# Optimization experiments

Measured on AMD Instinct MI355X. Metric: run time of the kernel, lower is better.

## Reference

```python
import jax, jax.numpy as jnp
import numpy as np

RCUT = 6.0      # cutoff radius
AXIS = 16       # axis_neuron
NORM = 64.0     # normalizer = avg_neighbors + 1 (precomputed stat)
EPS = 1e-15
NTYPES = 2


def _embed(h, W0, b0, W1, b1, W2, b2):
    # tiny per-type-pair embedding MLP: scalar sr -> C channels
    h = jnp.tanh(h @ W0 + b0)
    h = jnp.tanh(h @ W1 + b1)
    return jnp.tanh(h @ W2 + b2)


def _forward(coord_3N, box_33, srmean, srstd, xrsrstd, Gbias, Ebias,
             emb_W0, emb_b0, emb_W1, emb_b1, emb_W2, emb_b2,
             fit_W0, fit_b0, fit_W1, fit_b1, fit_W2, fit_b2, n1):
    N = coord_3N.shape[1]
    L = jnp.diagonal(box_33)  # orthorhombic box lengths (3,)
    # relative coords with minimum-image convention: x[d,i,j] = c[d,j] - c[d,i]
    x_3NM = coord_3N[:, None, :] - coord_3N[:, :, None]
    x_3NM = x_3NM - L[:, None, None] * jnp.round(x_3NM / L[:, None, None])
    eye = jnp.eye(N, dtype=bool)
    r_NM = jnp.sqrt(jnp.where(eye, 1.0, (x_3NM ** 2).sum(0)))  # diag masked for safe grad
    # smooth switching / r  (DeepPot-SE style sr)
    u = r_NM / RCUT
    sw = jnp.where((r_NM < RCUT) & (~eye), ((-6.0 * u + 15.0) * u - 10.0) * u ** 3 + 1.0, 0.0)
    sr_NM = sw / r_NM
    rsr_NM = sr_NM / r_NM
    idx = (0, n1, N)  # contiguous type boundaries (atoms sorted by type)
    rows_sr, rows_rsr, rows_emb = [], [], []
    for i in range(NTYPES):
        sr_i = sr_NM[idx[i]:idx[i + 1]]
        rows_sr.append(sr_i / srstd[i])
        rows_rsr.append(rsr_NM[idx[i]:idx[i + 1]] / xrsrstd[i])
        srn_i = (sr_i - srmean[i]) / srstd[i]
        blocks = []
        for j in range(NTYPES):
            p = NTYPES * i + j  # type-pair index
            blocks.append(_embed(srn_i[:, idx[j]:idx[j + 1], None],
                                 emb_W0[p], emb_b0[p], emb_W1[p], emb_b1[p], emb_W2[p], emb_b2[p]))
        rows_emb.append(jnp.concatenate(blocks, axis=1))
    srbias_NM = jnp.concatenate(rows_sr, axis=0)
    R_3NM = (jnp.concatenate(rows_rsr, axis=0)[None] + EPS) * x_3NM  # e3norm = 1
    embed_NMC = jnp.concatenate(rows_emb, axis=0)
    # weighted reductions over neighbor axis M (einsum avoids the 3*N*M*C temp)
    Ginv_NC = jnp.einsum('nm,nmc->nc', srbias_NM, embed_NMC) / NORM
    Geqv_3NC = jnp.einsum('dnm,nmc->dnc', R_3NM, embed_NMC) / NORM
    G_4NC = jnp.concatenate([(Ginv_NC + Gbias)[None], Geqv_3NC], axis=0)
    # equivariant outer-product descriptor: Feat[n,a,c] = sum_k G[k,n,c]*G[k,n,a]
    Feat_NX = jnp.einsum('knc,kna->nac', G_4NC, G_4NC[:, :, :AXIS]).reshape(N, -1)
    energy = jnp.zeros((), dtype=Feat_NX.dtype)
    for i in range(NTYPES):
        h = Feat_NX[idx[i]:idx[i + 1]]
        h = jnp.tanh(h @ fit_W0[i] + fit_b0[i])
        h = jnp.tanh(h @ fit_W1[i] + fit_b1[i])
        h = h @ fit_W2[i] + fit_b2[i]
        energy = energy + (h + Ebias[i]).sum()
    return energy


def setup_inputs() -> dict:
    key = jax.random.key(0)
    ks = jax.random.split(key, 20)
    N, N1, BOXL = 1024, 512, 20.0
    W = (16, 32, 64)
    X, F = AXIS * W[-1], 128

    def wt(k, shape, fan_in):
        return jax.random.normal(k, shape, jnp.float32) / np.float32(np.sqrt(fan_in))

    return {
        'coord_3N': jax.random.uniform(ks[0], (3, N), jnp.float32) * BOXL,
        'box_33': BOXL * jnp.eye(3, dtype=jnp.float32),
        'srmean': 0.1 * jax.random.uniform(ks[1], (NTYPES,), jnp.float32),
        'srstd': 0.5 + jax.random.uniform(ks[2], (NTYPES,), jnp.float32),
        'xrsrstd': 0.5 + jax.random.uniform(ks[3], (NTYPES,), jnp.float32),
        'Gbias': 0.1 * jax.random.normal(ks[4], (W[2],), jnp.float32),
        'Ebias': jax.random.normal(ks[5], (NTYPES,), jnp.float32),
        'emb_W0': wt(ks[6], (4, 1, W[0]), 1),
        'emb_b0': 0.1 * jax.random.normal(ks[7], (4, W[0]), jnp.float32),
        'emb_W1': wt(ks[8], (4, W[0], W[1]), W[0]),
        'emb_b1': 0.1 * jax.random.normal(ks[9], (4, W[1]), jnp.float32),
        'emb_W2': wt(ks[10], (4, W[1], W[2]), W[1]),
        'emb_b2': 0.1 * jax.random.normal(ks[11], (4, W[2]), jnp.float32),
        'fit_W0': wt(ks[12], (NTYPES, X, F), X),
        'fit_b0': 0.1 * jax.random.normal(ks[13], (NTYPES, F), jnp.float32),
        'fit_W1': wt(ks[14], (NTYPES, F, F), F),
        'fit_b1': 0.1 * jax.random.normal(ks[15], (NTYPES, F), jnp.float32),
        'fit_W2': wt(ks[16], (NTYPES, F, 1), F),
        'fit_b2': 0.1 * jax.random.normal(ks[17], (NTYPES, 1), jnp.float32),
        'n1': N1,
    }


def reference(coord_3N, box_33, srmean, srstd, xrsrstd, Gbias, Ebias,
              emb_W0, emb_b0, emb_W1, emb_b1, emb_W2, emb_b2,
              fit_W0, fit_b0, fit_W1, fit_b1, fit_W2, fit_b2, n1):
    return _forward(coord_3N, box_33, srmean, srstd, xrsrstd, Gbias, Ebias,
                    emb_W0, emb_b0, emb_W1, emb_b1, emb_W2, emb_b2,
                    fit_W0, fit_b0, fit_W1, fit_b1, fit_W2, fit_b2, n1)
```

## Files before the change

### kernel.cpp

```cpp
#include <hip/hip_runtime.h>

#define RCUT 6.0f

typedef _Float16 h2v __attribute__((ext_vector_type(2)));
typedef _Float16 h8  __attribute__((ext_vector_type(8)));
typedef float    f4  __attribute__((ext_vector_type(4)));

__device__ __forceinline__ float fast_tanh(float x) {
    float e = __expf(2.0f * x);
    return 1.0f - 2.0f * __builtin_amdgcn_rcpf(e + 1.0f);
}

__device__ __forceinline__ h2v pkh(float a, float b) {
#if __has_builtin(__builtin_amdgcn_cvt_pkrtz)
    union { __fp16 __attribute__((ext_vector_type(2))) r; h2v h; } u;
    u.r = __builtin_amdgcn_cvt_pkrtz(a, b);
    return u.h;
#else
    h2v r; r.x = (_Float16)a; r.y = (_Float16)b; return r;
#endif
}

__global__ __launch_bounds__(256, 3) void k_embed(
    const float* __restrict__ coord, const float* __restrict__ box,
    const float* __restrict__ srmean, const float* __restrict__ srstd,
    const float* __restrict__ xrsrstd, const float* __restrict__ Gbias,
    const float* __restrict__ eW0, const float* __restrict__ eb0,
    const float* __restrict__ eW1, const float* __restrict__ eb1,
    const float* __restrict__ eW2, const float* __restrict__ eb2,
    const int* __restrict__ n1p,
    const float* __restrict__ fW0, const float* __restrict__ fW1,
    h2v* __restrict__ feat, _Float16* __restrict__ W0ht,
    _Float16* __restrict__ W1ht, unsigned int* __restrict__ counter, int N)
{
    const int nb  = blockIdx.x;
    const int tid = threadIdx.x;
    const int NB  = N >> 1;

    __shared__ float s_w0[2][16], s_b0[2][16];
    __shared__ __align__(16) _Float16 s_srn[1024];
    __shared__ __align__(16) _Float16 s_cf[4][1024];
    __shared__ __align__(16) _Float16 s_h1[128][32];
    __shared__ __align__(16) _Float16 s_ef[4][4][64][8];
    __shared__ unsigned short s_nbr[1024];
    __shared__ float s_g4[2][256];
    __shared__ __align__(16) _Float16 w1t[2][32][24];
    __shared__ __align__(16) _Float16 w2t[2][64][40];
    __shared__ int s_wA[4], s_wB[4];

    if (nb >= NB) {
        const int b = nb - NB;
        if (b == 0 && tid == 0) *counter = 0u;
        float (*s_t)[33] = reinterpret_cast<float(*)[33]>(&s_ef[0][0][0][0]);
        if (b < 256) {
            int type = b >> 7, tb = b & 127;
            int ki = tb >> 2, ci = tb & 3;
            const float* src = fW0 + (size_t)type * 131072;
            int c = tid & 31, r0 = (tid >> 5) * 4;
            #pragma unroll
            for (int q = 0; q < 4; q++)
                s_t[r0 + q][c] = src[(size_t)(ki * 32 + r0 + q) * 128 + ci * 32 + c];
            __syncthreads();
            _Float16* dst = W0ht + (size_t)type * 131072;
            int kk = tid & 31, c0 = (tid >> 5) * 4;
            #pragma unroll
            for (int q = 0; q < 4; q++)
                dst[(size_t)(ci * 32 + c0 + q) * 1024 + ki * 32 + kk] = (_Float16)s_t[kk][c0 + q];
        } else {
            int b2v = b - 256, type = b2v >> 4, tb = b2v & 15;
            int ki = tb >> 2, ci = tb & 3;
            const float* src = fW1 + (size_t)type * 16384;
            int c = tid & 31, r0 = (tid >> 5) * 4;
            #pragma unroll
            for (int q = 0; q < 4; q++)
                s_t[r0 + q][c] = src[(size_t)(ki * 32 + r0 + q) * 128 + ci * 32 + c];
            __syncthreads();
            _Float16* dst = W1ht + (size_t)type * 16384;
            int kk = tid & 31, c0 = (tid >> 5) * 4;
            #pragma unroll
            for (int q = 0; q < 4; q++)
                dst[(size_t)(ci * 32 + c0 + q) * 128 + ki * 32 + kk] = (_Float16)s_t[kk][c0 + q];
        }
        return;
    }

    const int nA = 2 * nb, nBt = 2 * nb + 1;
    const int n1 = *n1p;
    const int ti = (nA >= n1) ? 1 : 0;
    const int wid = tid >> 6, lane = tid & 63;
    const int l15 = lane & 15, lk = lane >> 4;

    for (int t = tid; t < 32; t += 256) { int j = t >> 4, f = t & 15;
        s_w0[j][f] = eW0[(2 * ti + j) * 16 + f];
        s_b0[j][f] = eb0[(2 * ti + j) * 16 + f]; }
    for (int idx = tid; idx < 1024; idx += 256) {
        int j = idx >> 9, r = idx & 511, f = r >> 5, g = r & 31;
        w1t[j][g][f] = (_Float16)eW1[(2 * ti + j) * 512 + f * 32 + g];
    }
    for (int idx = tid; idx < 4096; idx += 256) {
        int j = idx >> 11, r = idx & 2047, g = r >> 6, c = r & 63;
        w2t[j][c][g] = (_Float16)eW2[(2 * ti + j) * 2048 + g * 64 + c];
    }
    float b1r[2][2], b2r[2][4];
    #pragma unroll
    for (int j = 0; j < 2; j++) {
        #pragma unroll
        for (int q = 0; q < 2; q++) b1r[j][q] = eb1[(2 * ti + j) * 32 + 16 * q + l15];
        #pragma unroll
        for (int q = 0; q < 4; q++) b2r[j][q] = eb2[(2 * ti + j) * 64 + 16 * q + l15];
    }

    const float Lx = box[0], Ly = box[4], Lz = box[8];
    const float iLx = 1.0f / Lx, iLy = 1.0f / Ly, iLz = 1.0f / Lz;
    const float xA = coord[nA], yA = coord[N + nA], zA = coord[2 * N + nA];
    const float xB = coord[nBt], yB = coord[N + nBt], zB = coord[2 * N + nBt];
    const float srm  = srmean[ti];
    const float isrs = 1.0f / srstd[ti];
    const float ixrs = 1.0f / xrsrstd[ti];

    unsigned long long balA[4], balB[4];
    float dxA[4], dyA[4], dzA[4], r2A[4];
    float dxB[4], dyB[4], dzB[4], r2B[4];
    {
        int wA = 0, wB = 0;
        const int mystart = wid * 256;
        #pragma unroll
        for (int r = 0; r < 4; r++) {
            int m = mystart + r * 64 + lane;
            float x = coord[m], y = coord[N + m], z = coord[2 * N + m];
            float ax = x - xA; ax -= Lx * rintf(ax * iLx);
            float ay = y - yA; ay -= Ly * rintf(ay * iLy);
            float az = z - zA; az -= Lz * rintf(az * iLz);
            float ra = ax * ax + ay * ay + az * az;
            float bx = x - xB; bx -= Lx * rintf(bx * iLx);
            float by = y - yB; by -= Ly * rintf(by * iLy);
            float bz = z - zB; bz -= Lz * rintf(bz * iLz);
            float rb = bx * bx + by * by + bz * bz;
            dxA[r] = ax; dyA[r] = ay; dzA[r] = az; r2A[r] = ra;
            dxB[r] = bx; dyB[r] = by; dzB[r] = bz; r2B[r] = rb;
            bool pA = (ra < RCUT * RCUT) && (m != nA);
            bool pB = (rb < RCUT * RCUT) && (m != nBt);
            balA[r] = __ballot(pA);
            balB[r] = __ballot(pB);
            wA += (int)__popcll(balA[r]);
            wB += (int)__popcll(balB[r]);
        }
        if (lane == 0) { s_wA[wid] = wA; s_wB[wid] = wB; }
    }
    __syncthreads();
    int cntA = s_wA[0] + s_wA[1] + s_wA[2] + s_wA[3];
    int cntB = s_wB[0] + s_wB[1] + s_wB[2] + s_wB[3];
    int cnt  = cntA + cntB;
    if (cnt > 1024) cnt = 1024;
    if (cntA > 1024) cntA = 1024;
    {
        int baseA = 0, baseB = cntA;
        for (int w = 0; w < wid; w++) { baseA += s_wA[w]; baseB += s_wB[w]; }
        const unsigned long long lt = (1ull << lane) - 1ull;
        const int mystart = wid * 256;
        #pragma unroll
        for (int r = 0; r < 4; r++) {
            int m = mystart + r * 64 + lane;
            #pragma unroll
            for (int cc = 0; cc < 2; cc++) {
                unsigned long long bal = cc ? balB[r] : balA[r];
                int base = cc ? baseB : baseA;
                if ((bal >> lane) & 1ull) {
                    int pos = base + (int)__popcll(bal & lt);
                    if (pos < 1024) {
                        float dx = cc ? dxB[r] : dxA[r];
                        float dy = cc ? dyB[r] : dyA[r];
                        float dz = cc ? dzB[r] : dzA[r];
                        float r2 = cc ? r2B[r] : r2A[r];
                        float rr = sqrtf(r2);
                        float rinv = __builtin_amdgcn_rcpf(rr);
                        float u  = rr * (1.0f / RCUT);
                        float u3 = u * u * u;
                        float sw_ = ((-6.0f * u + 15.0f) * u - 10.0f) * u3 + 1.0f;
                        float sr  = sw_ * rinv;
                        float crs = sr * rinv * ixrs + 1e-15f;
                        s_srn[pos]   = (_Float16)((sr - srm) * isrs);
                        s_cf[0][pos] = (_Float16)(sr * isrs);
                        s_cf[1][pos] = (_Float16)(crs * dx);
                        s_cf[2][pos] = (_Float16)(crs * dy);
                        s_cf[3][pos] = (_Float16)(crs * dz);
                        s_nbr[pos]   = (unsigned short)m;
                    }
                }
                if (cc) baseB += (int)__popcll(bal);
                else    baseA += (int)__popcll(bal);
            }
        }
    }
    __syncthreads();
    const int ntiles = (cnt + 127) >> 7;
    for (int i = cnt + tid; i < ntiles * 128; i += 256) {
        s_srn[i] = (_Float16)0.0f; s_nbr[i] = 0;
        s_cf[0][i] = (_Float16)0.0f; s_cf[1][i] = (_Float16)0.0f;
        s_cf[2][i] = (_Float16)0.0f; s_cf[3][i] = (_Float16)0.0f;
    }
    __syncthreads();

    f4 gacc = {0.0f, 0.0f, 0.0f, 0.0f};
    const f4 zf4 = {0.0f, 0.0f, 0.0f, 0.0f};

    for (int t = 0; t < ntiles; t++) {
        const int t128 = t << 7;
        __syncthreads();

        #pragma unroll
        for (int mt2 = 0; mt2 < 2; mt2++) {
            const int mt = 2 * wid + mt2;
            const int row = 16 * mt + l15;
            const int rp = t128 + row;
            float srn = (float)s_srn[rp];
            int jr = (s_nbr[rp] >= n1) ? 1 : 0;
            h8 a = {};
            if (lk < 2) {
                const float* wp = &s_w0[jr][8 * lk];
                const float* bp = &s_b0[jr][8 * lk];
                #pragma unroll
                for (int q = 0; q < 8; q++)
                    a[q] = (_Float16)fast_tanh(fmaf(srn, wp[q], bp[q]));
            }
            #pragma unroll
            for (int nt1 = 0; nt1 < 2; nt1++) {
                const int c = 16 * nt1 + l15;
                h8 b0f = {}, b1f = {};
                if (lk < 2) {
                    b0f = *(const h8*)&w1t[0][c][8 * lk];
                    b1f = *(const h8*)&w1t[1][c][8 * lk];
                }
                f4 d0 = __builtin_amdgcn_mfma_f32_16x16x32_f16(a, b0f, zf4, 0, 0, 0);
                f4 d1 = __builtin_amdgcn_mfma_f32_16x16x32_f16(a, b1f, zf4, 0, 0, 0);
                #pragma unroll
                for (int r = 0; r < 4; r++) {
                    int gp = 16 * mt + 4 * lk + r;
                    bool is0 = (s_nbr[t128 + gp] < n1);
                    float hv = fast_tanh((is0 ? d0[r] : d1[r]) + (is0 ? b1r[0][nt1] : b1r[1][nt1]));
                    int e = 16 * nt1 + l15;
                    s_h1[gp][(((e >> 3) ^ ((gp >> 1) & 3)) << 3) + (e & 7)] = (_Float16)hv;
                }
            }
        }
        asm volatile("" ::: "memory");
        #pragma unroll
        for (int mt2 = 0; mt2 < 2; mt2++) {
            const int mt = 2 * wid + mt2;
            const int row = 16 * mt + l15;
            h8 a2 = *(const h8*)&s_h1[row][((lk ^ ((row >> 1) & 3)) << 3)];
            #pragma unroll
            for (int nt = 0; nt < 4; nt++) {
                const int c = 16 * nt + l15;
                h8 w20 = *(const h8*)&w2t[0][c][8 * lk];
                h8 w21 = *(const h8*)&w2t[1][c][8 * lk];
                f4 e0 = __builtin_amdgcn_mfma_f32_16x16x32_f16(a2, w20, zf4, 0, 0, 0);
                f4 e1 = __builtin_amdgcn_mfma_f32_16x16x32_f16(a2, w21, zf4, 0, 0, 0);
                #pragma unroll
                for (int r = 0; r < 4; r++) {
                    int gp = 16 * mt + 4 * lk + r;
                    bool is0 = (s_nbr[t128 + gp] < n1);
                    float ev = fast_tanh((is0 ? e0[r] : e1[r]) + (is0 ? b2r[0][nt] : b2r[1][nt]));
                    s_ef[nt][gp >> 5][l15 + 16 * ((gp & 31) >> 3)][gp & 7] = (_Float16)ev;
                }
            }
        }
        __syncthreads();

        #pragma unroll
        for (int ks = 0; ks < 4; ks++) {
            const int s = t128 + 32 * ks;
            h8 ac = {};
            if (l15 < 8) {
                const bool rowA = l15 < 4;
                const int  cr   = rowA ? l15 : (l15 - 4);
                const bool allA = (s + 31) < cntA;
                const bool allB = s >= cntA;
                if ((allA && rowA) || (allB && !rowA)) {
                    ac = *(const h8*)&s_cf[cr][s + 8 * lk];
                } else if (!allA && !allB) {
                    #pragma unroll
                    for (int r = 0; r < 8; r++) {
                        int p = s + 8 * lk + r;
                        bool isA = p < cntA;
                        if (isA == rowA) ac[r] = s_cf[cr][p];
                    }
                }
            }
            h8 eb = *(const h8*)&s_ef[wid][ks][lane][0];
            gacc = __builtin_amdgcn_mfma_f32_16x16x32_f16(ac, eb, gacc, 0, 0, 0);
        }
    }

    if (lk < 2) {
        float* sg = &s_g4[lk][0];
        #pragma unroll
        for (int r = 0; r < 4; r++) {
            float gv = gacc[r] * (1.0f / 64.0f);
            if (r == 0) gv += Gbias[16 * wid + l15];
            sg[r * 64 + 16 * wid + l15] = gv;
        }
    }
    __syncthreads();
    #pragma unroll
    for (int at = 0; at < 2; at++) {
        const float* sg = &s_g4[at][0];
        h2v* outp = feat + (size_t)(2 * nb + at) * 512;
        #pragma unroll
        for (int q = 0; q < 2; q++) {
            int o2 = tid + 256 * q;
            int a = o2 >> 5, c = (2 * o2) & 63;
            float ga0 = sg[a],       ga1 = sg[64 + a];
            float ga2 = sg[128 + a], ga3 = sg[192 + a];
            float s0 = ga0 * sg[c];
            s0 = fmaf(ga1, sg[64 + c],  s0);
            s0 = fmaf(ga2, sg[128 + c], s0);
            s0 = fmaf(ga3, sg[192 + c], s0);
            float s1 = ga0 * sg[c + 1];
            s1 = fmaf(ga1, sg[64 + c + 1],  s1);
            s1 = fmaf(ga2, sg[128 + c + 1], s1);
            s1 = fmaf(ga3, sg[192 + c + 1], s1);
            outp[o2] = pkh(s0, s1);
        }
    }
}

__global__ __launch_bounds__(512, 1) void k_fit(
    const _Float16* __restrict__ featf, const _Float16* __restrict__ W0ht,
    const _Float16* __restrict__ W1ht,
    const float* __restrict__ b0, const float* __restrict__ b1,
    const float* __restrict__ W2, const float* __restrict__ b2,
    const float* __restrict__ Ebias, const int* __restrict__ n1p,
    unsigned int* __restrict__ counter, float* __restrict__ slots,
    float* __restrict__ out)
{
    __shared__ float s_red[4][2][16][64];
    __shared__ __align__(16) _Float16 s_hd[16][128];
    __shared__ float s_sum[16][32];

    const int tid = threadIdx.x;
    const int lane = tid & 63, w = tid >> 6;
    const int kq = w >> 1, ch = w & 1;
    const int l15 = lane & 15, lk = lane >> 4;
    const int n0 = blockIdx.x * 16;
    const int ia = (n0 >= *n1p) ? 1 : 0;
    const f4 zf4 = {0.0f, 0.0f, 0.0f, 0.0f};

    const _Float16* Ap = featf + (size_t)(n0 + l15) * 1024 + kq * 256;
    const _Float16* B0 = W0ht + (size_t)ia * 131072 + kq * 256;
    f4 acc[4] = {zf4, zf4, zf4, zf4};
    #pragma unroll
    for (int ks = 0; ks < 8; ks++) {
        h8 a = *(const h8*)(Ap + ks * 32 + 8 * lk);
        #pragma unroll
        for (int nt = 0; nt < 4; nt++) {
            const int c = ch * 64 + nt * 16 + l15;
            h8 b = *(const h8*)(B0 + (size_t)c * 1024 + ks * 32 + 8 * lk);
            acc[nt] = __builtin_amdgcn_mfma_f32_16x16x32_f16(a, b, acc[nt], 0, 0, 0);
        }
    }
    #pragma unroll
    for (int nt = 0; nt < 4; nt++)
        #pragma unroll
        for (int r = 0; r < 4; r++)
            s_red[kq][ch][4 * lk + r][nt * 16 + l15] = acc[nt][r];
    __syncthreads();

    {
        const int row = tid >> 5, c0 = (tid & 31) * 4;
        const int chh = c0 >> 6, cl = c0 & 63;
        f4 v = *(const f4*)&s_red[0][chh][row][cl];
        v += *(const f4*)&s_red[1][chh][row][cl];
        v += *(const f4*)&s_red[2][chh][row][cl];
        v += *(const f4*)&s_red[3][chh][row][cl];
        #pragma unroll
        for (int q = 0; q < 4; q++) {
            int c = c0 + q;
            float h = fast_tanh(v[q] + b0[ia * 128 + c]);
            s_hd[row][(((c >> 3) ^ row) << 3) + (c & 7)] = (_Float16)h;
        }
    }
    __syncthreads();

    f4 acc1[4] = {zf4, zf4, zf4, zf4};
    {
        h8 a = *(const h8*)&s_hd[l15][(((4 * kq + lk) ^ l15) & 15) << 3];
        const _Float16* B1 = W1ht + (size_t)ia * 16384 + kq * 32;
        #pragma unroll
        for (int nt = 0; nt < 4; nt++) {
            const int c = ch * 64 + nt * 16 + l15;
            h8 b = *(const h8*)(B1 + (size_t)c * 128 + 8 * lk);
            acc1[nt] = __builtin_amdgcn_mfma_f32_16x16x32_f16(a, b, zf4, 0, 0, 0);
        }
    }
    #pragma unroll
    for (int nt = 0; nt < 4; nt++)
        #pragma unroll
        for (int r = 0; r < 4; r++)
            s_red[kq][ch][4 * lk + r][nt * 16 + l15] = acc1[nt][r];
    __syncthreads();

    {
        const int row = tid >> 5, c0 = (tid & 31) * 4;
        const int chh = c0 >> 6, cl = c0 & 63;
        f4 v = *(const f4*)&s_red[0][chh][row][cl];
        v += *(const f4*)&s_red[1][chh][row][cl];
        v += *(const f4*)&s_red[2][chh][row][cl];
        v += *(const f4*)&s_red[3][chh][row][cl];
        float pv = 0.0f;
        #pragma unroll
        for (int q = 0; q < 4; q++) {
            int c = c0 + q;
            pv += fast_tanh(v[q] + b1[ia * 128 + c]) * W2[ia * 128 + c];
        }
        s_sum[row][tid & 31] = pv;
    }
    __syncthreads();
    if (w == 0) {
        const int row = lane >> 2, g = lane & 3;
        float s = 0.0f;
        #pragma unroll
        for (int i = 0; i < 8; i++) s += s_sum[row][8 * g + i];
        s += __shfl_xor(s, 1);  s += __shfl_xor(s, 2);
        s += __shfl_xor(s, 4);  s += __shfl_xor(s, 8);
        s += __shfl_xor(s, 16); s += __shfl_xor(s, 32);
        if (lane == 0) {
            float e = s + 16.0f * (b2[ia] + Ebias[ia]);
            slots[blockIdx.x] = e;
            __threadfence();
            unsigned int old = atomicAdd(counter, 1u);
            if (old == 63u) {
                __threadfence();
                float tot = 0.0f;
                for (int i = 0; i < 64; i++)
                    tot += __hip_atomic_load(&slots[i], __ATOMIC_RELAXED, __HIP_MEMORY_SCOPE_AGENT);
                out[0] = tot;
            }
        }
    }
}

extern "C" void kernel_launch(void* const* d_in, const int* in_sizes, int n_in,
                              void* d_out, int out_size, void* d_ws, size_t ws_size,
                              hipStream_t stream) {
    const float* coord   = (const float*)d_in[0];
    const float* box     = (const float*)d_in[1];
    const float* srmean  = (const float*)d_in[2];
    const float* srstd   = (const float*)d_in[3];
    const float* xrsrstd = (const float*)d_in[4];
    const float* Gbias   = (const float*)d_in[5];
    const float* Ebias   = (const float*)d_in[6];
    const float* eW0     = (const float*)d_in[7];
    const float* eb0     = (const float*)d_in[8];
    const float* eW1     = (const float*)d_in[9];
    const float* eb1     = (const float*)d_in[10];
    const float* eW2     = (const float*)d_in[11];
    const float* eb2     = (const float*)d_in[12];
    const float* fW0     = (const float*)d_in[13];
    const float* fb0     = (const float*)d_in[14];
    const float* fW1     = (const float*)d_in[15];
    const float* fb1     = (const float*)d_in[16];
    const float* fW2     = (const float*)d_in[17];
    const float* fb2     = (const float*)d_in[18];
    const int*   n1p     = (const int*)d_in[19];

    const int N = in_sizes[0] / 3;
    h2v*      featbuf = (h2v*)d_ws;
    _Float16* W0ht = (_Float16*)((char*)d_ws + (size_t)2 * 1024 * 1024);
    _Float16* W1ht = W0ht + 2 * 131072;
    char* tail = (char*)d_ws + (size_t)(2 * 1024 + 512 + 64) * 1024;
    unsigned int* counter = (unsigned int*)tail;
    float*        slots   = (float*)(tail + 64);

    k_embed<<<N / 2 + 288, 256, 0, stream>>>(coord, box, srmean, srstd, xrsrstd,
                                             Gbias, eW0, eb0, eW1, eb1, eW2, eb2,
                                             n1p, fW0, fW1, featbuf, W0ht, W1ht,
                                             counter, N);
    k_fit<<<N / 16, 512, 0, stream>>>((const _Float16*)featbuf, W0ht, W1ht,
                                      fb0, fb1, fW2, fb2, Ebias, n1p,
                                      counter, slots, (float*)d_out);
}
```

Baseline: 39.42 us.

## Keep embedding weights in registers and accumulate G per-warp in 16-row chunks

Moves the embedding MLP weights from shared-memory tables into per-lane MFMA fragment registers. The neighbor list is restructured into 16-row chunks with A and B atoms padded separately. Each warp processes chunks independently and accumulates the weighted G reductions in FP32 registers, replacing the per-128-tile block barriers and the final MFMA reduction. Cross-warp sums go through a small shared buffer. This removes most __syncthreads and LDS weight traffic, but raises register pressure, adds scalar FMA work, and caps A neighbors at 512.

```diff
diff --git a/kernel.cpp b/kernel.cpp
--- a/kernel.cpp
+++ b/kernel.cpp
@@ -37,21 +37,19 @@
     const int tid = threadIdx.x;
     const int NB  = N >> 1;
 
-    __shared__ float s_w0[2][16], s_b0[2][16];
-    __shared__ __align__(16) _Float16 s_srn[1024];
-    __shared__ __align__(16) _Float16 s_cf[4][1024];
-    __shared__ __align__(16) _Float16 s_h1[128][32];
-    __shared__ __align__(16) _Float16 s_ef[4][4][64][8];
+    __shared__ float s_srn[1024];
+    __shared__ __align__(16) float s_cf[4][1024];
     __shared__ unsigned short s_nbr[1024];
+    __shared__ __align__(16) _Float16 s_h1w[4][16][36];
+    __shared__ float s_gA[4][4][64];
+    __shared__ float s_gB[4][4][64];
     __shared__ float s_g4[2][256];
-    __shared__ __align__(16) _Float16 w1t[2][32][24];
-    __shared__ __align__(16) _Float16 w2t[2][64][40];
     __shared__ int s_wA[4], s_wB[4];
 
     if (nb >= NB) {
         const int b = nb - NB;
         if (b == 0 && tid == 0) *counter = 0u;
-        float (*s_t)[33] = reinterpret_cast<float(*)[33]>(&s_ef[0][0][0][0]);
+        float (*s_t)[33] = reinterpret_cast<float(*)[33]>(&s_cf[0][0]);
         if (b < 256) {
             int type = b >> 7, tb = b & 127;
             int ki = tb >> 2, ci = tb & 3;
@@ -90,24 +88,50 @@
     const int wid = tid >> 6, lane = tid & 63;
     const int l15 = lane & 15, lk = lane >> 4;
 
-    for (int t = tid; t < 32; t += 256) { int j = t >> 4, f = t & 15;
-        s_w0[j][f] = eW0[(2 * ti + j) * 16 + f];
-        s_b0[j][f] = eb0[(2 * ti + j) * 16 + f]; }
-    for (int idx = tid; idx < 1024; idx += 256) {
-        int j = idx >> 9, r = idx & 511, f = r >> 5, g = r & 31;
-        w1t[j][g][f] = (_Float16)eW1[(2 * ti + j) * 512 + f * 32 + g];
-    }
-    for (int idx = tid; idx < 4096; idx += 256) {
-        int j = idx >> 11, r = idx & 2047, g = r >> 6, c = r & 63;
-        w2t[j][c][g] = (_Float16)eW2[(2 * ti + j) * 2048 + g * 64 + c];
-    }
-    float b1r[2][2], b2r[2][4];
+    h8 w0h[2], b0h[2];
     #pragma unroll
     for (int j = 0; j < 2; j++) {
-        #pragma unroll
-        for (int q = 0; q < 2; q++) b1r[j][q] = eb1[(2 * ti + j) * 32 + 16 * q + l15];
-        #pragma unroll
-        for (int q = 0; q < 4; q++) b2r[j][q] = eb2[(2 * ti + j) * 64 + 16 * q + l15];
+        h8 wv = {}, bv = {};
+        if (lk < 2) {
+            #pragma unroll
+            for (int q = 0; q < 8; q++) {
+                wv[q] = (_Float16)eW0[(2 * ti + j) * 16 + 8 * lk + q];
+                bv[q] = (_Float16)eb0[(2 * ti + j) * 16 + 8 * lk + q];
+            }
+        }
+        w0h[j] = wv; b0h[j] = bv;
+    }
+    h8 w1f[2][2];
+    float b1r[2][2];
+    #pragma unroll
+    for (int j = 0; j < 2; j++) {
+        const float* w1g = eW1 + (size_t)(2 * ti + j) * 512;
+        #pragma unroll
+        for (int nt1 = 0; nt1 < 2; nt1++) {
+            h8 v = {};
+            if (lk < 2) {
+                #pragma unroll
+                for (int r = 0; r < 8; r++)
+                    v[r] = (_Float16)w1g[(8 * lk + r) * 32 + 16 * nt1 + l15];
+            }
+            w1f[j][nt1] = v;
+            b1r[j][nt1] = eb1[(2 * ti + j) * 32 + 16 * nt1 + l15];
+        }
+    }
+    h8 w2f[2][4];
+    float b2r[2][4];
+    #pragma unroll
+    for (int j = 0; j < 2; j++) {
+        const float* w2g = eW2 + (size_t)(2 * ti + j) * 2048;
+        #pragma unroll
+        for (int nt = 0; nt < 4; nt++) {
+            h8 v;
+            #pragma unroll
+            for (int r = 0; r < 8; r++)
+                v[r] = (_Float16)w2g[(8 * lk + r) * 64 + 16 * nt + l15];
+            w2f[j][nt] = v;
+            b2r[j][nt] = eb2[(2 * ti + j) * 64 + 16 * nt + l15];
+        }
     }
 
     const float Lx = box[0], Ly = box[4], Lz = box[8];
@@ -150,11 +174,23 @@
     __syncthreads();
     int cntA = s_wA[0] + s_wA[1] + s_wA[2] + s_wA[3];
     int cntB = s_wB[0] + s_wB[1] + s_wB[2] + s_wB[3];
-    int cnt  = cntA + cntB;
-    if (cnt > 1024) cnt = 1024;
-    if (cntA > 1024) cntA = 1024;
+    if (cntA > 512) cntA = 512;
+    const int cntA_pad = (cntA + 15) & ~15;
+    if (cntB > 1024 - cntA_pad) cntB = 1024 - cntA_pad;
+    const int cntB_pad = (cntB + 15) & ~15;
+    const int nchunks = (cntA_pad + cntB_pad) >> 4;
+
     {
-        int baseA = 0, baseB = cntA;
+        f4 z = {0.f, 0.f, 0.f, 0.f};
+        *(f4*)&s_srn[tid * 4] = z;
+        #pragma unroll
+        for (int k = 0; k < 4; k++) *(f4*)&s_cf[k][tid * 4] = z;
+        *(unsigned long long*)&s_nbr[tid * 4] = 0ull;
+    }
+    __syncthreads();
+
+    {
+        int baseA = 0, baseB = cntA_pad;
         for (int w = 0; w < wid; w++) { baseA += s_wA[w]; baseB += s_wB[w]; }
         const unsigned long long lt = (1ull << lane) - 1ull;
         const int mystart = wid * 256;
@@ -165,9 +201,10 @@
             for (int cc = 0; cc < 2; cc++) {
                 unsigned long long bal = cc ? balB[r] : balA[r];
                 int base = cc ? baseB : baseA;
+                int lim  = cc ? (cntA_pad + cntB) : cntA;
                 if ((bal >> lane) & 1ull) {
                     int pos = base + (int)__popcll(bal & lt);
-                    if (pos < 1024) {
+                    if (pos < lim) {
                         float dx = cc ? dxB[r] : dxA[r];
                         float dy = cc ? dyB[r] : dyA[r];
                         float dz = cc ? dzB[r] : dzA[r];
@@ -179,11 +216,11 @@
                         float sw_ = ((-6.0f * u + 15.0f) * u - 10.0f) * u3 + 1.0f;
                         float sr  = sw_ * rinv;
                         float crs = sr * rinv * ixrs + 1e-15f;
-                        s_srn[pos]   = (_Float16)((sr - srm) * isrs);
-                        s_cf[0][pos] = (_Float16)(sr * isrs);
-                        s_cf[1][pos] = (_Float16)(crs * dx);
-                        s_cf[2][pos] = (_Float16)(crs * dy);
-                        s_cf[3][pos] = (_Float16)(crs * dz);
+                        s_srn[pos]   = (sr - srm) * isrs;
+                        s_cf[0][pos] = sr * isrs;
+                        s_cf[1][pos] = crs * dx;
+                        s_cf[2][pos] = crs * dy;
+                        s_cf[3][pos] = crs * dz;
                         s_nbr[pos]   = (unsigned short)m;
                     }
                 }
@@ -193,115 +230,102 @@
         }
     }
     __syncthreads();
-    const int ntiles = (cnt + 127) >> 7;
-    for (int i = cnt + tid; i < ntiles * 128; i += 256) {
-        s_srn[i] = (_Float16)0.0f; s_nbr[i] = 0;
-        s_cf[0][i] = (_Float16)0.0f; s_cf[1][i] = (_Float16)0.0f;
-        s_cf[2][i] = (_Float16)0.0f; s_cf[3][i] = (_Float16)0.0f;
-    }
-    __syncthreads();
-
-    f4 gacc = {0.0f, 0.0f, 0.0f, 0.0f};
+
     const f4 zf4 = {0.0f, 0.0f, 0.0f, 0.0f};
-
-    for (int t = 0; t < ntiles; t++) {
-        const int t128 = t << 7;
-        __syncthreads();
-
-        #pragma unroll
-        for (int mt2 = 0; mt2 < 2; mt2++) {
-            const int mt = 2 * wid + mt2;
-            const int row = 16 * mt + l15;
-            const int rp = t128 + row;
-            float srn = (float)s_srn[rp];
-            int jr = (s_nbr[rp] >= n1) ? 1 : 0;
-            h8 a = {};
-            if (lk < 2) {
-                const float* wp = &s_w0[jr][8 * lk];
-                const float* bp = &s_b0[jr][8 * lk];
+    float gkA[4][4] = {}, gkB[4][4] = {};
+
+    for (int ch = wid; ch < nchunks; ch += 4) {
+        const int base = ch << 4;
+        const bool isB = base >= cntA_pad;
+
+        float srn = s_srn[base + l15];
+        int jrow = (s_nbr[base + l15] >= n1) ? 1 : 0;
+        h8 a = {};
+        if (lk < 2) {
+            #pragma unroll
+            for (int q = 0; q < 8; q++) {
+                float wv = jrow ? (float)w0h[1][q] : (float)w0h[0][q];
+                float bv = jrow ? (float)b0h[1][q] : (float)b0h[0][q];
+                a[q] = (_Float16)fast_tanh(fmaf(srn, wv, bv));
+            }
+        }
+        int j_r[4];
+        #pragma unroll
+        for (int r = 0; r < 4; r++)
+            j_r[r] = (s_nbr[base + 4 * lk + r] >= n1) ? 1 : 0;
+
+        #pragma unroll
+        for (int nt1 = 0; nt1 < 2; nt1++) {
+            f4 d0 = __builtin_amdgcn_mfma_f32_16x16x32_f16(a, w1f[0][nt1], zf4, 0, 0, 0);
+            f4 d1 = __builtin_amdgcn_mfma_f32_16x16x32_f16(a, w1f[1][nt1], zf4, 0, 0, 0);
+            #pragma unroll
+            for (int r = 0; r < 4; r++) {
+                float dv = j_r[r] ? d1[r] : d0[r];
+                float bv = j_r[r] ? b1r[1][nt1] : b1r[0][nt1];
+                s_h1w[wid][4 * lk + r][16 * nt1 + l15] = (_Float16)fast_tanh(dv + bv);
+            }
+        }
+        asm volatile("" ::: "memory");
+        h8 a2 = *(const h8*)&s_h1w[wid][l15][8 * lk];
+
+        f4 cfv[4];
+        #pragma unroll
+        for (int k = 0; k < 4; k++)
+            cfv[k] = *(const f4*)&s_cf[k][base + 4 * lk];
+
+        #pragma unroll
+        for (int nt = 0; nt < 4; nt++) {
+            f4 e0 = __builtin_amdgcn_mfma_f32_16x16x32_f16(a2, w2f[0][nt], zf4, 0, 0, 0);
+            f4 e1 = __builtin_amdgcn_mfma_f32_16x16x32_f16(a2, w2f[1][nt], zf4, 0, 0, 0);
+            float ev[4];
+            #pragma unroll
+            for (int r = 0; r < 4; r++) {
+                float dv = j_r[r] ? e1[r] : e0[r];
+                float bv = j_r[r] ? b2r[1][nt] : b2r[0][nt];
+                ev[r] = fast_tanh(dv + bv);
+            }
+            if (isB) {
                 #pragma unroll
-                for (int q = 0; q < 8; q++)
-                    a[q] = (_Float16)fast_tanh(fmaf(srn, wp[q], bp[q]));
-            }
-            #pragma unroll
-            for (int nt1 = 0; nt1 < 2; nt1++) {
-                const int c = 16 * nt1 + l15;
-                h8 b0f = {}, b1f = {};
-                if (lk < 2) {
-                    b0f = *(const h8*)&w1t[0][c][8 * lk];
-                    b1f = *(const h8*)&w1t[1][c][8 * lk];
-                }
-                f4 d0 = __builtin_amdgcn_mfma_f32_16x16x32_f16(a, b0f, zf4, 0, 0, 0);
-                f4 d1 = __builtin_amdgcn_mfma_f32_16x16x32_f16(a, b1f, zf4, 0, 0, 0);
+                for (int k = 0; k < 4; k++)
+                    #pragma unroll
+                    for (int r = 0; r < 4; r++)
+                        gkB[k][nt] = fmaf(cfv[k][r], ev[r], gkB[k][nt]);
+            } else {
                 #pragma unroll
-                for (int r = 0; r < 4; r++) {
-                    int gp = 16 * mt + 4 * lk + r;
-                    bool is0 = (s_nbr[t128 + gp] < n1);
-                    float hv = fast_tanh((is0 ? d0[r] : d1[r]) + (is0 ? b1r[0][nt1] : b1r[1][nt1]));
-                    int e = 16 * nt1 + l15;
-                    s_h1[gp][(((e >> 3) ^ ((gp >> 1) & 3)) << 3) + (e & 7)] = (_Float16)hv;
-                }
-            }
-        }
-        asm volatile("" ::: "memory");
-        #pragma unroll
-        for (int mt2 = 0; mt2 < 2; mt2++) {
-            const int mt = 2 * wid + mt2;
-            const int row = 16 * mt + l15;
-            h8 a2 = *(const h8*)&s_h1[row][((lk ^ ((row >> 1) & 3)) << 3)];
-            #pragma unroll
-            for (int nt = 0; nt < 4; nt++) {
-                const int c = 16 * nt + l15;
-                h8 w20 = *(const h8*)&w2t[0][c][8 * lk];
-                h8 w21 = *(const h8*)&w2t[1][c][8 * lk];
-                f4 e0 = __builtin_amdgcn_mfma_f32_16x16x32_f16(a2, w20, zf4, 0, 0, 0);
-                f4 e1 = __builtin_amdgcn_mfma_f32_16x16x32_f16(a2, w21, zf4, 0, 0, 0);
-                #pragma unroll
-                for (int r = 0; r < 4; r++) {
-                    int gp = 16 * mt + 4 * lk + r;
-                    bool is0 = (s_nbr[t128 + gp] < n1);
-                    float ev = fast_tanh((is0 ? e0[r] : e1[r]) + (is0 ? b2r[0][nt] : b2r[1][nt]));
-                    s_ef[nt][gp >> 5][l15 + 16 * ((gp & 31) >> 3)][gp & 7] = (_Float16)ev;
-                }
-            }
-        }
-        __syncthreads();
-
-        #pragma unroll
-        for (int ks = 0; ks < 4; ks++) {
-            const int s = t128 + 32 * ks;
-            h8 ac = {};
-            if (l15 < 8) {
-                const bool rowA = l15 < 4;
-                const int  cr   = rowA ? l15 : (l15 - 4);
-                const bool allA = (s + 31) < cntA;
-                const bool allB = s >= cntA;
-                if ((allA && rowA) || (allB && !rowA)) {
-                    ac = *(const h8*)&s_cf[cr][s + 8 * lk];
-                } else if (!allA && !allB) {
+                for (int k = 0; k < 4; k++)
                     #pragma unroll
-                    for (int r = 0; r < 8; r++) {
-                        int p = s + 8 * lk + r;
-                        bool isA = p < cntA;
-                        if (isA == rowA) ac[r] = s_cf[cr][p];
-                    }
-                }
-            }
-            h8 eb = *(const h8*)&s_ef[wid][ks][lane][0];
-            gacc = __builtin_amdgcn_mfma_f32_16x16x32_f16(ac, eb, gacc, 0, 0, 0);
-        }
-    }
-
-    if (lk < 2) {
-        float* sg = &s_g4[lk][0];
-        #pragma unroll
-        for (int r = 0; r < 4; r++) {
-            float gv = gacc[r] * (1.0f / 64.0f);
-            if (r == 0) gv += Gbias[16 * wid + l15];
-            sg[r * 64 + 16 * wid + l15] = gv;
-        }
-    }
-    __syncthreads();
+                    for (int r = 0; r < 4; r++)
+                        gkA[k][nt] = fmaf(cfv[k][r], ev[r], gkA[k][nt]);
+            }
+        }
+    }
+
+    #pragma unroll
+    for (int k = 0; k < 4; k++) {
+        #pragma unroll
+        for (int nt = 0; nt < 4; nt++) {
+            float vA = gkA[k][nt], vB = gkB[k][nt];
+            vA += __shfl_xor(vA, 16); vA += __shfl_xor(vA, 32);
+            vB += __shfl_xor(vB, 16); vB += __shfl_xor(vB, 32);
+            if (lane < 16) {
+                s_gA[wid][k][nt * 16 + lane] = vA;
+                s_gB[wid][k][nt * 16 + lane] = vB;
+            }
+        }
+    }
+    __syncthreads();
+    #pragma unroll
+    for (int it = 0; it < 2; it++) {
+        int idx = tid + 256 * it;
+        int at = idx >> 8, k = (idx >> 6) & 3, c = idx & 63;
+        const float (*sg)[4][64] = at ? s_gB : s_gA;
+        float g = (sg[0][k][c] + sg[1][k][c]) + (sg[2][k][c] + sg[3][k][c]);
+        g *= (1.0f / 64.0f);
+        if (k == 0) g += Gbias[c];
+        s_g4[at][k * 64 + c] = g;
+    }
+    __syncthreads();
+
     #pragma unroll
     for (int at = 0; at < 2; at++) {
         const float* sg = &s_g4[at][0];
@@ -309,9 +333,9 @@
         #pragma unroll
         for (int q = 0; q < 2; q++) {
             int o2 = tid + 256 * q;
-            int a = o2 >> 5, c = (2 * o2) & 63;
-            float ga0 = sg[a],       ga1 = sg[64 + a];
-            float ga2 = sg[128 + a], ga3 = sg[192 + a];
+            int aa = o2 >> 5, c = (2 * o2) & 63;
+            float ga0 = sg[aa],       ga1 = sg[64 + aa];
+            float ga2 = sg[128 + aa], ga3 = sg[192 + aa];
             float s0 = ga0 * sg[c];
             s0 = fmaf(ga1, sg[64 + c],  s0);
             s0 = fmaf(ga2, sg[128 + c], s0);
```

New measurement: 42.76 us. 8.5% more time.
